# Kernel tuning notes

Hardware: AMD Instinct MI355X
Metric: run time of the kernel (lower is better)

## Reference

```python
import jax, jax.numpy as jnp
import numpy as np

SEQ_LEN = 4096
D_IN = 1024
D_OUT = 1024


def setup_inputs() -> dict:
    key = jax.random.key(0)
    k_x, k_q, k_k, k_v = jax.random.split(key, 4)
    s = 1.0 / np.sqrt(D_IN)
    return {
        "x": jax.random.normal(k_x, (SEQ_LEN, D_IN), dtype=jnp.float32),
        "W_query": jax.random.normal(k_q, (D_IN, D_OUT), dtype=jnp.float32) * s,
        "W_key": jax.random.normal(k_k, (D_IN, D_OUT), dtype=jnp.float32) * s,
        "W_value": jax.random.normal(k_v, (D_IN, D_OUT), dtype=jnp.float32) * s,
    }


def reference(x, W_query, W_key, W_value):
    # QKV projections (Linear without bias): [S, d_out]
    q = x @ W_query
    k = x @ W_key
    v = x @ W_value
    # Full S x S score matrix, causal mask, scaled softmax
    scores = q @ k.T  # [S, S]
    seq_len = x.shape[0]
    causal = jnp.tril(jnp.ones((seq_len, seq_len), dtype=bool))
    scores = jnp.where(causal, scores, -jnp.inf)
    scale = 1.0 / jnp.sqrt(jnp.asarray(k.shape[-1], dtype=scores.dtype))
    attn = jax.nn.softmax(scores * scale, axis=-1)
    return attn @ v  # [S, d_out]
```

## Files before the change

kernel.cpp:

```cpp
#include <hip/hip_runtime.h>
#include <math.h>

#define SEQ 4096
#define DIM 1024

typedef unsigned short u16;
typedef __attribute__((ext_vector_type(8))) short short8;
typedef __attribute__((ext_vector_type(4))) float floatx4;
typedef __attribute__((ext_vector_type(4))) unsigned short us4;

__device__ __forceinline__ float bf2f(u16 u) {
    union { unsigned int i; float f; } c; c.i = ((unsigned int)u) << 16; return c.f;
}
__device__ __forceinline__ u16 f2bf(float f) {
    union { float f; unsigned int i; } c; c.f = f;
    return (u16)((c.i + 0x7fffu + ((c.i >> 16) & 1u)) >> 16);
}
__device__ __forceinline__ void gload_lds16(const u16* g, u16* l) {
    __builtin_amdgcn_global_load_lds((const __attribute__((address_space(1))) void*)g,
                                     (__attribute__((address_space(3))) void*)l, 16, 0, 0);
}

__device__ __forceinline__ void tile64(const u16* __restrict__ A,
                                       const u16* __restrict__ B,
                                       u16 (&As)[3][2048], u16 (&Bs)[3][2048],
                                       int lda, int ldb,
                                       int row0, int col0, int kend,
                                       int wave, int lane,
                                       floatx4 (&acc)[2][2]) {
    const int wm = wave & 1, wn = wave >> 1;
    const int s0 = wave * 64 + lane;
    const int r0 = s0 >> 2, q0 = ((s0 & 3) ^ ((s0 >> 3) & 3)) * 8;
    const u16* aP = A + (size_t)(row0 + r0) * lda + q0;
    const u16* bP = B + (size_t)(col0 + r0) * ldb + q0;
    const int l0 = wave * 512;
    const int frow = lane & 15;
    const int xq = (((lane >> 4) ^ ((frow >> 1) & 3))) * 8;
    const int mrow0 = wm * 32, nrow0 = wn * 32;
    const int niter = kend >> 5;

    gload_lds16(aP, &As[0][l0]); gload_lds16(bP, &Bs[0][l0]); aP += 32; bP += 32;
    gload_lds16(aP, &As[1][l0]); gload_lds16(bP, &Bs[1][l0]); aP += 32; bP += 32;

    int cur = 0, pre = 2;
    for (int it = 0; it < niter - 2; ++it) {
        asm volatile("s_waitcnt vmcnt(2)\n\ts_barrier" ::: "memory");
        short8 af[2], bfr[2];
#pragma unroll
        for (int t = 0; t < 2; ++t) {
            af[t]  = *(const short8*)&As[cur][(mrow0 + t * 16 + frow) * 32 + xq];
            bfr[t] = *(const short8*)&Bs[cur][(nrow0 + t * 16 + frow) * 32 + xq];
        }
        gload_lds16(aP, &As[pre][l0]); gload_lds16(bP, &Bs[pre][l0]);
        aP += 32; bP += 32;
#pragma unroll
        for (int mt = 0; mt < 2; ++mt)
#pragma unroll
            for (int nt = 0; nt < 2; ++nt)
                acc[mt][nt] = __builtin_amdgcn_mfma_f32_16x16x32_bf16(
                    af[mt], bfr[nt], acc[mt][nt], 0, 0, 0);
        cur = (cur == 2) ? 0 : cur + 1;
        pre = (pre == 2) ? 0 : pre + 1;
    }
#pragma unroll
    for (int fin = 0; fin < 2; ++fin) {
        if (fin == 0)
            asm volatile("s_waitcnt vmcnt(2)\n\ts_barrier" ::: "memory");
        else
            asm volatile("s_waitcnt vmcnt(0)\n\ts_barrier" ::: "memory");
        short8 af[2], bfr[2];
#pragma unroll
        for (int t = 0; t < 2; ++t) {
            af[t]  = *(const short8*)&As[cur][(mrow0 + t * 16 + frow) * 32 + xq];
            bfr[t] = *(const short8*)&Bs[cur][(nrow0 + t * 16 + frow) * 32 + xq];
        }
#pragma unroll
        for (int mt = 0; mt < 2; ++mt)
#pragma unroll
            for (int nt = 0; nt < 2; ++nt)
                acc[mt][nt] = __builtin_amdgcn_mfma_f32_16x16x32_bf16(
                    af[mt], bfr[nt], acc[mt][nt], 0, 0, 0);
        cur = (cur == 2) ? 0 : cur + 1;
    }
}

__global__ __launch_bounds__(256) void gemm128(const u16* __restrict__ A,
                                               const u16* __restrict__ B,
                                               u16* __restrict__ Cout,
                                               u16* __restrict__ VtOut,
                                               int lda, int ldb, int ldc, int Kdim,
                                               float scale0) {
    const int row0 = blockIdx.y * 128;
    const int col0 = blockIdx.x * 128;

    __shared__ u16 As[3][4096];
    __shared__ u16 Bs[3][4096];

    const int tid  = threadIdx.x;
    const int wave = tid >> 6;
    const int lane = tid & 63;
    const int wm = wave & 1;
    const int wn = wave >> 1;

    const int s0 = wave * 128 + lane;
    const int s1 = s0 + 64;
    const int r0s = s0 >> 2, q0s = ((s0 & 3) ^ ((s0 >> 3) & 3)) * 8;
    const int r1s = s1 >> 2, q1s = ((s1 & 3) ^ ((s1 >> 3) & 3)) * 8;
    const u16* aP0 = A + (size_t)(row0 + r0s) * lda + q0s;
    const u16* aP1 = A + (size_t)(row0 + r1s) * lda + q1s;
    const u16* bP0 = B + (size_t)(col0 + r0s) * ldb + q0s;
    const u16* bP1 = B + (size_t)(col0 + r1s) * ldb + q1s;
    const int l0 = wave * 1024;

    floatx4 acc[4][4] = {};
    const int niter = Kdim >> 5;
    const int frow = lane & 15;
    const int xq = (((lane >> 4) ^ ((frow >> 1) & 3))) * 8;

    auto stage = [&](int c) {
        gload_lds16(aP0, &As[c][l0]);
        gload_lds16(aP1, &As[c][l0 + 512]);
        gload_lds16(bP0, &Bs[c][l0]);
        gload_lds16(bP1, &Bs[c][l0 + 512]);
        aP0 += 32; aP1 += 32; bP0 += 32; bP1 += 32;
    };
    stage(0);
    stage(1);

    auto compute_tile = [&](int c) {
        short8 af[4], bfr[4];
#pragma unroll
        for (int t = 0; t < 4; ++t) {
            af[t]  = *(const short8*)&As[c][(wm * 64 + t * 16 + frow) * 32 + xq];
            bfr[t] = *(const short8*)&Bs[c][(wn * 64 + t * 16 + frow) * 32 + xq];
        }
#pragma unroll
        for (int mt = 0; mt < 4; ++mt)
#pragma unroll
            for (int nt = 0; nt < 4; ++nt)
                acc[mt][nt] = __builtin_amdgcn_mfma_f32_16x16x32_bf16(
                    af[mt], bfr[nt], acc[mt][nt], 0, 0, 0);
    };

    int cur = 0, pre = 2;
    for (int it = 0; it < niter - 2; ++it) {
        asm volatile("s_waitcnt vmcnt(4)\n\ts_barrier" ::: "memory");
        short8 af[4], bfr[4];
#pragma unroll
        for (int t = 0; t < 4; ++t) {
            af[t]  = *(const short8*)&As[cur][(wm * 64 + t * 16 + frow) * 32 + xq];
            bfr[t] = *(const short8*)&Bs[cur][(wn * 64 + t * 16 + frow) * 32 + xq];
        }
        stage(pre);
#pragma unroll
        for (int mt = 0; mt < 4; ++mt)
#pragma unroll
            for (int nt = 0; nt < 4; ++nt)
                acc[mt][nt] = __builtin_amdgcn_mfma_f32_16x16x32_bf16(
                    af[mt], bfr[nt], acc[mt][nt], 0, 0, 0);
        cur = (cur == 2) ? 0 : cur + 1;
        pre = (pre == 2) ? 0 : pre + 1;
    }
    asm volatile("s_waitcnt vmcnt(4)\n\ts_barrier" ::: "memory");
    compute_tile(cur);
    cur = (cur == 2) ? 0 : cur + 1;
    asm volatile("s_waitcnt vmcnt(0)\n\ts_barrier" ::: "memory");
    compute_tile(cur);

    const int cr = (lane >> 4) * 4;
    const int cc = lane & 15;
    if (col0 >= 2048) {
#pragma unroll
        for (int mt = 0; mt < 4; ++mt)
#pragma unroll
            for (int nt = 0; nt < 4; ++nt) {
                const int row = row0 + wm * 64 + mt * 16 + cr;
                const int col = (col0 - 2048) + wn * 64 + nt * 16 + cc;
                us4 o = { f2bf(acc[mt][nt][0]), f2bf(acc[mt][nt][1]),
                          f2bf(acc[mt][nt][2]), f2bf(acc[mt][nt][3]) };
                *(us4*)&VtOut[(size_t)col * SEQ + row] = o;
            }
    } else {
        const float sc = (col0 < 1024) ? scale0 : 1.0f;
#pragma unroll
        for (int mt = 0; mt < 4; ++mt)
#pragma unroll
            for (int nt = 0; nt < 4; ++nt)
#pragma unroll
                for (int r = 0; r < 4; ++r) {
                    const int row = row0 + wm * 64 + mt * 16 + cr + r;
                    const int col = col0 + wn * 64 + nt * 16 + cc;
                    Cout[(size_t)row * ldc + col] = f2bf(acc[mt][nt][r] * sc);
                }
    }
}

__global__ __launch_bounds__(256) void scores64(const u16* __restrict__ QK,
                                                u16* __restrict__ E,
                                                float* __restrict__ Lsum) {
    const int t = blockIdx.x;
    int by = (int)((sqrtf(8.0f * t + 1.0f) - 1.0f) * 0.5f);
    while ((by + 1) * (by + 2) / 2 <= t) ++by;
    while (by * (by + 1) / 2 > t) --by;
    const int bx = t - by * (by + 1) / 2;
    const int row0 = by * 64, col0 = bx * 64;

    __shared__ u16 As[3][2048], Bs[3][2048];
    const int tid = threadIdx.x, wave = tid >> 6, lane = tid & 63;

    floatx4 acc[2][2] = {};
    tile64(QK, QK + 1024, As, Bs, 2048, 2048, row0, col0, DIM, wave, lane, acc);

    const int wm = wave & 1, wn = wave >> 1;
    const int cr = (lane >> 4) * 4, cc = lane & 15;
#pragma unroll
    for (int mt = 0; mt < 2; ++mt) {
#pragma unroll
        for (int r = 0; r < 4; ++r) {
            const int grow = row0 + wm * 32 + mt * 16 + cr + r;
            float rowsum = 0.f;
#pragma unroll
            for (int nt = 0; nt < 2; ++nt) {
                const int gcol = col0 + wn * 32 + nt * 16 + cc;
                const float e = (gcol <= grow) ? __expf(acc[mt][nt][r]) : 0.f;
                rowsum += e;
                E[(size_t)grow * SEQ + gcol] = f2bf(e);
            }
            rowsum += __shfl_xor(rowsum, 1);
            rowsum += __shfl_xor(rowsum, 2);
            rowsum += __shfl_xor(rowsum, 4);
            rowsum += __shfl_xor(rowsum, 8);
            if (cc == 0) atomicAdd(&Lsum[grow], rowsum);
        }
    }
}

__global__ __launch_bounds__(256) void pv64(const u16* __restrict__ E,
                                            const u16* __restrict__ Vt,
                                            float* __restrict__ O,
                                            const float* __restrict__ Lsum,
                                            unsigned* __restrict__ Tick) {
    __shared__ u16 As[3][2048], Bs[3][2048];
    __shared__ unsigned sh_t;
    const int tid = threadIdx.x, wave = tid >> 6, lane = tid & 63;
    const int wm = wave & 1, wn = wave >> 1;
    const int cr = (lane >> 4) * 4, cc = lane & 15;

    for (;;) {
        if (tid == 0) sh_t = atomicAdd(Tick, 1u);
        __syncthreads();
        const unsigned t = sh_t;
        if (t >= 1024u) return;
        const int r = 63 - (int)(t >> 4);
        const int x = (int)(t & 15u);
        const int row0 = r * 64, col0 = x * 64;

        floatx4 acc[2][2] = {};
        tile64(E, Vt, As, Bs, SEQ, SEQ, row0, col0, row0 + 64, wave, lane, acc);

#pragma unroll
        for (int mt = 0; mt < 2; ++mt)
#pragma unroll
            for (int rr = 0; rr < 4; ++rr) {
                const int grow = row0 + wm * 32 + mt * 16 + cr + rr;
                const float invl = __builtin_amdgcn_rcpf(Lsum[grow]);
#pragma unroll
                for (int nt = 0; nt < 2; ++nt) {
                    const int col = col0 + wn * 32 + nt * 16 + cc;
                    O[(size_t)grow * DIM + col] = acc[mt][nt][rr] * invl;
                }
            }
    }
}

__global__ __launch_bounds__(256) void prep(const float* __restrict__ x,
                                            const float* __restrict__ W0,
                                            const float* __restrict__ W1,
                                            const float* __restrict__ W2,
                                            u16* __restrict__ xb,
                                            u16* __restrict__ Wt,
                                            float* __restrict__ Lsum,
                                            unsigned* __restrict__ Tick) {
    __shared__ float tile[32][33];
    const int b = blockIdx.x;
    const int tid = threadIdx.x;
    if (b < 4096) {
        const size_t i = ((size_t)b * 256 + tid) * 4;
        const float4 v = *(const float4*)(x + i);
        us4 o = { f2bf(v.x), f2bf(v.y), f2bf(v.z), f2bf(v.w) };
        *(us4*)(xb + i) = o;
    } else if (b < 7168) {
        const int t = b - 4096;
        const int z = t >> 10;
        const int idx = t & 1023;
        const float* W = (z == 0) ? W0 : (z == 1) ? W1 : W2;
        u16* out = Wt + (size_t)z * DIM * DIM;
        const int bx = (idx & 31) * 32;
        const int by = (idx >> 5) * 32;
        const int tx = tid & 31;
        const int ty = (tid >> 5) * 4;
#pragma unroll
        for (int r = 0; r < 4; ++r)
            tile[ty + r][tx] = W[(size_t)(by + ty + r) * DIM + bx + tx];
        __syncthreads();
#pragma unroll
        for (int r = 0; r < 4; ++r)
            out[(size_t)(bx + ty + r) * DIM + by + tx] = f2bf(tile[tx][ty + r]);
    } else {
        const int t = b - 7168;
        *(float4*)(Lsum + (size_t)(t * 256 + tid) * 4) =
            make_float4(0.f, 0.f, 0.f, 0.f);
        if (t == 0 && tid == 0) *Tick = 0u;
    }
}

extern "C" void kernel_launch(void* const* d_in, const int* in_sizes, int n_in,
                              void* d_out, int out_size, void* d_ws, size_t ws_size,
                              hipStream_t stream) {
    const float* x  = (const float*)d_in[0];
    const float* Wq = (const float*)d_in[1];
    const float* Wk = (const float*)d_in[2];
    const float* Wv = (const float*)d_in[3];

    u16* xb    = (u16*)d_ws;
    u16* Wt    = xb  + (size_t)SEQ * DIM;
    u16* QK    = Wt  + (size_t)3072 * DIM;
    u16* Vt    = QK  + (size_t)SEQ * 2048;
    u16* E     = Vt  + (size_t)DIM * SEQ;
    float* Lsum = (float*)(E + (size_t)SEQ * SEQ);
    unsigned* Tick = (unsigned*)(Lsum + SEQ);

    prep<<<7172, 256, 0, stream>>>(x, Wq, Wk, Wv, xb, Wt, Lsum, Tick);

    gemm128<<<dim3(24, 32), 256, 0, stream>>>(
        xb, Wt, QK, Vt, DIM, DIM, 2048, DIM, 0.03125f);

    scores64<<<2080, 256, 0, stream>>>(QK, E, Lsum);

    pv64<<<768, 256, 0, stream>>>(E, Vt, (float*)d_out, Lsum, Tick);
}
```

Before: 220.9 us.

## Split V projection into scores kernel, use 128 score tiles, static PV schedule

Q/K projection now runs alone, and the V projection is merged into the scores kernel so the two run side by side. Score tiles grow from 64 to 128 (528 causal tiles instead of 2080), which improves data reuse. The PV kernel drops its atomic work-stealing ticket for a fixed interleaved mapping that pairs heavy and light rows. The risks are load imbalance from the static schedule and fewer, larger blocks in the scores stage.

```diff
diff --git a/kernel.cpp b/kernel.cpp
--- a/kernel.cpp
+++ b/kernel.cpp
@@ -21,87 +21,13 @@
                                      (__attribute__((address_space(3))) void*)l, 16, 0, 0);
 }
 
-__device__ __forceinline__ void tile64(const u16* __restrict__ A,
-                                       const u16* __restrict__ B,
-                                       u16 (&As)[3][2048], u16 (&Bs)[3][2048],
-                                       int lda, int ldb,
-                                       int row0, int col0, int kend,
-                                       int wave, int lane,
-                                       floatx4 (&acc)[2][2]) {
+__device__ __forceinline__ void pipe128(const u16* __restrict__ A,
+                                        const u16* __restrict__ B,
+                                        u16 (&As)[3][4096], u16 (&Bs)[3][4096],
+                                        int lda, int ldb, int row0, int col0,
+                                        int wave, int lane,
+                                        floatx4 (&acc)[4][4]) {
     const int wm = wave & 1, wn = wave >> 1;
-    const int s0 = wave * 64 + lane;
-    const int r0 = s0 >> 2, q0 = ((s0 & 3) ^ ((s0 >> 3) & 3)) * 8;
-    const u16* aP = A + (size_t)(row0 + r0) * lda + q0;
-    const u16* bP = B + (size_t)(col0 + r0) * ldb + q0;
-    const int l0 = wave * 512;
-    const int frow = lane & 15;
-    const int xq = (((lane >> 4) ^ ((frow >> 1) & 3))) * 8;
-    const int mrow0 = wm * 32, nrow0 = wn * 32;
-    const int niter = kend >> 5;
-
-    gload_lds16(aP, &As[0][l0]); gload_lds16(bP, &Bs[0][l0]); aP += 32; bP += 32;
-    gload_lds16(aP, &As[1][l0]); gload_lds16(bP, &Bs[1][l0]); aP += 32; bP += 32;
-
-    int cur = 0, pre = 2;
-    for (int it = 0; it < niter - 2; ++it) {
-        asm volatile("s_waitcnt vmcnt(2)\n\ts_barrier" ::: "memory");
-        short8 af[2], bfr[2];
-#pragma unroll
-        for (int t = 0; t < 2; ++t) {
-            af[t]  = *(const short8*)&As[cur][(mrow0 + t * 16 + frow) * 32 + xq];
-            bfr[t] = *(const short8*)&Bs[cur][(nrow0 + t * 16 + frow) * 32 + xq];
-        }
-        gload_lds16(aP, &As[pre][l0]); gload_lds16(bP, &Bs[pre][l0]);
-        aP += 32; bP += 32;
-#pragma unroll
-        for (int mt = 0; mt < 2; ++mt)
-#pragma unroll
-            for (int nt = 0; nt < 2; ++nt)
-                acc[mt][nt] = __builtin_amdgcn_mfma_f32_16x16x32_bf16(
-                    af[mt], bfr[nt], acc[mt][nt], 0, 0, 0);
-        cur = (cur == 2) ? 0 : cur + 1;
-        pre = (pre == 2) ? 0 : pre + 1;
-    }
-#pragma unroll
-    for (int fin = 0; fin < 2; ++fin) {
-        if (fin == 0)
-            asm volatile("s_waitcnt vmcnt(2)\n\ts_barrier" ::: "memory");
-        else
-            asm volatile("s_waitcnt vmcnt(0)\n\ts_barrier" ::: "memory");
-        short8 af[2], bfr[2];
-#pragma unroll
-        for (int t = 0; t < 2; ++t) {
-            af[t]  = *(const short8*)&As[cur][(mrow0 + t * 16 + frow) * 32 + xq];
-            bfr[t] = *(const short8*)&Bs[cur][(nrow0 + t * 16 + frow) * 32 + xq];
-        }
-#pragma unroll
-        for (int mt = 0; mt < 2; ++mt)
-#pragma unroll
-            for (int nt = 0; nt < 2; ++nt)
-                acc[mt][nt] = __builtin_amdgcn_mfma_f32_16x16x32_bf16(
-                    af[mt], bfr[nt], acc[mt][nt], 0, 0, 0);
-        cur = (cur == 2) ? 0 : cur + 1;
-    }
-}
-
-__global__ __launch_bounds__(256) void gemm128(const u16* __restrict__ A,
-                                               const u16* __restrict__ B,
-                                               u16* __restrict__ Cout,
-                                               u16* __restrict__ VtOut,
-                                               int lda, int ldb, int ldc, int Kdim,
-                                               float scale0) {
-    const int row0 = blockIdx.y * 128;
-    const int col0 = blockIdx.x * 128;
-
-    __shared__ u16 As[3][4096];
-    __shared__ u16 Bs[3][4096];
-
-    const int tid  = threadIdx.x;
-    const int wave = tid >> 6;
-    const int lane = tid & 63;
-    const int wm = wave & 1;
-    const int wn = wave >> 1;
-
     const int s0 = wave * 128 + lane;
     const int s1 = s0 + 64;
     const int r0s = s0 >> 2, q0s = ((s0 & 3) ^ ((s0 >> 3) & 3)) * 8;
@@ -111,9 +37,6 @@
     const u16* bP0 = B + (size_t)(col0 + r0s) * ldb + q0s;
     const u16* bP1 = B + (size_t)(col0 + r1s) * ldb + q1s;
     const int l0 = wave * 1024;
-
-    floatx4 acc[4][4] = {};
-    const int niter = Kdim >> 5;
     const int frow = lane & 15;
     const int xq = (((lane >> 4) ^ ((frow >> 1) & 3))) * 8;
 
@@ -143,7 +66,7 @@
     };
 
     int cur = 0, pre = 2;
-    for (int it = 0; it < niter - 2; ++it) {
+    for (int it = 0; it < 30; ++it) {
         asm volatile("s_waitcnt vmcnt(4)\n\ts_barrier" ::: "memory");
         short8 af[4], bfr[4];
 #pragma unroll
@@ -166,71 +89,89 @@
     cur = (cur == 2) ? 0 : cur + 1;
     asm volatile("s_waitcnt vmcnt(0)\n\ts_barrier" ::: "memory");
     compute_tile(cur);
-
-    const int cr = (lane >> 4) * 4;
-    const int cc = lane & 15;
-    if (col0 >= 2048) {
+}
+
+__global__ __launch_bounds__(256) void projQK(const u16* __restrict__ xb,
+                                              const u16* __restrict__ Wt,
+                                              u16* __restrict__ QK,
+                                              float scale0) {
+    __shared__ u16 As[3][4096], Bs[3][4096];
+    const int row0 = blockIdx.y * 128;
+    const int col0 = blockIdx.x * 128;
+    const int tid = threadIdx.x, wave = tid >> 6, lane = tid & 63;
+    const int wm = wave & 1, wn = wave >> 1;
+
+    floatx4 acc[4][4] = {};
+    pipe128(xb, Wt, As, Bs, DIM, DIM, row0, col0, wave, lane, acc);
+
+    const int cr = (lane >> 4) * 4, cc = lane & 15;
+    const float sc = (col0 < 1024) ? scale0 : 1.0f;
+#pragma unroll
+    for (int mt = 0; mt < 4; ++mt)
+#pragma unroll
+        for (int nt = 0; nt < 4; ++nt)
+#pragma unroll
+            for (int r = 0; r < 4; ++r) {
+                const int row = row0 + wm * 64 + mt * 16 + cr + r;
+                const int col = col0 + wn * 64 + nt * 16 + cc;
+                QK[(size_t)row * 2048 + col] = f2bf(acc[mt][nt][r] * sc);
+            }
+}
+
+__global__ __launch_bounds__(256) void scoresV(const u16* __restrict__ QK,
+                                               const u16* __restrict__ xb,
+                                               const u16* __restrict__ Wt,
+                                               u16* __restrict__ E,
+                                               u16* __restrict__ Vt,
+                                               float* __restrict__ Lsum) {
+    __shared__ u16 As[3][4096], Bs[3][4096];
+    const int t = blockIdx.x;
+    const int tid = threadIdx.x, wave = tid >> 6, lane = tid & 63;
+    const int wm = wave & 1, wn = wave >> 1;
+    const int cr = (lane >> 4) * 4, cc = lane & 15;
+
+    floatx4 acc[4][4] = {};
+    if (t < 256) {
+        const int row0 = (t >> 3) * 128;
+        const int colv = (t & 7) * 128;
+        pipe128(xb, Wt, As, Bs, DIM, DIM, row0, 2048 + colv, wave, lane, acc);
 #pragma unroll
         for (int mt = 0; mt < 4; ++mt)
 #pragma unroll
             for (int nt = 0; nt < 4; ++nt) {
                 const int row = row0 + wm * 64 + mt * 16 + cr;
-                const int col = (col0 - 2048) + wn * 64 + nt * 16 + cc;
+                const int col = colv + wn * 64 + nt * 16 + cc;
                 us4 o = { f2bf(acc[mt][nt][0]), f2bf(acc[mt][nt][1]),
                           f2bf(acc[mt][nt][2]), f2bf(acc[mt][nt][3]) };
-                *(us4*)&VtOut[(size_t)col * SEQ + row] = o;
+                *(us4*)&Vt[(size_t)col * SEQ + row] = o;
             }
     } else {
-        const float sc = (col0 < 1024) ? scale0 : 1.0f;
-#pragma unroll
-        for (int mt = 0; mt < 4; ++mt)
-#pragma unroll
-            for (int nt = 0; nt < 4; ++nt)
-#pragma unroll
-                for (int r = 0; r < 4; ++r) {
-                    const int row = row0 + wm * 64 + mt * 16 + cr + r;
-                    const int col = col0 + wn * 64 + nt * 16 + cc;
-                    Cout[(size_t)row * ldc + col] = f2bf(acc[mt][nt][r] * sc);
+        const int s = t - 256;
+        int by = (int)((sqrtf(8.0f * s + 1.0f) - 1.0f) * 0.5f);
+        while ((by + 1) * (by + 2) / 2 <= s) ++by;
+        while (by * (by + 1) / 2 > s) --by;
+        const int bx = s - by * (by + 1) / 2;
+        const int row0 = by * 128, col0 = bx * 128;
+        pipe128(QK, QK + 1024, As, Bs, 2048, 2048, row0, col0, wave, lane, acc);
+#pragma unroll
+        for (int mt = 0; mt < 4; ++mt) {
+#pragma unroll
+            for (int r = 0; r < 4; ++r) {
+                const int grow = row0 + wm * 64 + mt * 16 + cr + r;
+                float rowsum = 0.f;
+#pragma unroll
+                for (int nt = 0; nt < 4; ++nt) {
+                    const int gcol = col0 + wn * 64 + nt * 16 + cc;
+                    const float e = (gcol <= grow) ? __expf(acc[mt][nt][r]) : 0.f;
+                    rowsum += e;
+                    E[(size_t)grow * SEQ + gcol] = f2bf(e);
                 }
-    }
-}
-
-__global__ __launch_bounds__(256) void scores64(const u16* __restrict__ QK,
-                                                u16* __restrict__ E,
-                                                float* __restrict__ Lsum) {
-    const int t = blockIdx.x;
-    int by = (int)((sqrtf(8.0f * t + 1.0f) - 1.0f) * 0.5f);
-    while ((by + 1) * (by + 2) / 2 <= t) ++by;
-    while (by * (by + 1) / 2 > t) --by;
-    const int bx = t - by * (by + 1) / 2;
-    const int row0 = by * 64, col0 = bx * 64;
-
-    __shared__ u16 As[3][2048], Bs[3][2048];
-    const int tid = threadIdx.x, wave = tid >> 6, lane = tid & 63;
-
-    floatx4 acc[2][2] = {};
-    tile64(QK, QK + 1024, As, Bs, 2048, 2048, row0, col0, DIM, wave, lane, acc);
-
-    const int wm = wave & 1, wn = wave >> 1;
-    const int cr = (lane >> 4) * 4, cc = lane & 15;
-#pragma unroll
-    for (int mt = 0; mt < 2; ++mt) {
-#pragma unroll
-        for (int r = 0; r < 4; ++r) {
-            const int grow = row0 + wm * 32 + mt * 16 + cr + r;
-            float rowsum = 0.f;
-#pragma unroll
-            for (int nt = 0; nt < 2; ++nt) {
-                const int gcol = col0 + wn * 32 + nt * 16 + cc;
-                const float e = (gcol <= grow) ? __expf(acc[mt][nt][r]) : 0.f;
-                rowsum += e;
-                E[(size_t)grow * SEQ + gcol] = f2bf(e);
+                rowsum += __shfl_xor(rowsum, 1);
+                rowsum += __shfl_xor(rowsum, 2);
+                rowsum += __shfl_xor(rowsum, 4);
+                rowsum += __shfl_xor(rowsum, 8);
+                if (cc == 0) atomicAdd(&Lsum[grow], rowsum);
             }
-            rowsum += __shfl_xor(rowsum, 1);
-            rowsum += __shfl_xor(rowsum, 2);
-            rowsum += __shfl_xor(rowsum, 4);
-            rowsum += __shfl_xor(rowsum, 8);
-            if (cc == 0) atomicAdd(&Lsum[grow], rowsum);
         }
     }
 }
@@ -238,39 +179,101 @@
 __global__ __launch_bounds__(256) void pv64(const u16* __restrict__ E,
                                             const u16* __restrict__ Vt,
                                             float* __restrict__ O,
-                                            const float* __restrict__ Lsum,
-                                            unsigned* __restrict__ Tick) {
+                                            const float* __restrict__ Lsum) {
+    const int lin = blockIdx.x + (blockIdx.y << 4);
+    const int c = lin & 7;
+    const int j = lin >> 3;
+    const int x = j & 15;
+    const int m = j >> 4;
+    const unsigned long long PK = 0x2F3F20301F0F1000ULL;
+    const int base = (int)((PK >> (m * 8)) & 0x3F);
+    const int r = base + ((m & 2) ? -c : c);
+    const int row0 = r * 64;
+    const int col0 = x * 64;
+    const int kend = row0 + 64;
+
     __shared__ u16 As[3][2048], Bs[3][2048];
-    __shared__ unsigned sh_t;
-    const int tid = threadIdx.x, wave = tid >> 6, lane = tid & 63;
-    const int wm = wave & 1, wn = wave >> 1;
+
+    const int tid  = threadIdx.x;
+    const int wave = tid >> 6;
+    const int lane = tid & 63;
+    const int wm = wave & 1;
+    const int wn = wave >> 1;
+
+    const int s0 = wave * 64 + lane;
+    const int r0 = s0 >> 2, q0 = ((s0 & 3) ^ ((s0 >> 3) & 3)) * 8;
+    const u16* aP = E  + (size_t)(row0 + r0) * SEQ + q0;
+    const u16* bP = Vt + (size_t)(col0 + r0) * SEQ + q0;
+    const int l0 = wave * 512;
+
+    floatx4 acc[2][2] = {};
+    const int niter = kend >> 5;
+    const int frow = lane & 15;
+    const int xq = (((lane >> 4) ^ ((frow >> 1) & 3))) * 8;
+    const int mrow0 = wm * 32, nrow0 = wn * 32;
+
+    auto stage = [&](int cb) {
+        gload_lds16(aP, &As[cb][l0]);
+        gload_lds16(bP, &Bs[cb][l0]);
+        aP += 32; bP += 32;
+    };
+    stage(0);
+    stage(1);
+
+    auto compute_tile = [&](int cb) {
+        short8 af[2], bfr[2];
+#pragma unroll
+        for (int t = 0; t < 2; ++t) {
+            af[t]  = *(const short8*)&As[cb][(mrow0 + t * 16 + frow) * 32 + xq];
+            bfr[t] = *(const short8*)&Bs[cb][(nrow0 + t * 16 + frow) * 32 + xq];
+        }
+#pragma unroll
+        for (int mt = 0; mt < 2; ++mt)
+#pragma unroll
+            for (int nt = 0; nt < 2; ++nt)
+                acc[mt][nt] = __builtin_amdgcn_mfma_f32_16x16x32_bf16(
+                    af[mt], bfr[nt], acc[mt][nt], 0, 0, 0);
+    };
+
+    int cur = 0, pre = 2;
+    for (int it = 0; it < niter - 2; ++it) {
+        asm volatile("s_waitcnt vmcnt(2)\n\ts_barrier" ::: "memory");
+        short8 af[2], bfr[2];
+#pragma unroll
+        for (int t = 0; t < 2; ++t) {
+            af[t]  = *(const short8*)&As[cur][(mrow0 + t * 16 + frow) * 32 + xq];
+            bfr[t] = *(const short8*)&Bs[cur][(nrow0 + t * 16 + frow) * 32 + xq];
+        }
+        stage(pre);
+#pragma unroll
+        for (int mt = 0; mt < 2; ++mt)
+#pragma unroll
+            for (int nt = 0; nt < 2; ++nt)
+                acc[mt][nt] = __builtin_amdgcn_mfma_f32_16x16x32_bf16(
+                    af[mt], bfr[nt], acc[mt][nt], 0, 0, 0);
+        cur = (cur == 2) ? 0 : cur + 1;
+        pre = (pre == 2) ? 0 : pre + 1;
+    }
+    asm volatile("s_waitcnt vmcnt(2)\n\ts_barrier" ::: "memory");
+    compute_tile(cur);
+    cur = (cur == 2) ? 0 : cur + 1;
+    asm volatile("s_waitcnt vmcnt(0)\n\ts_barrier" ::: "memory");
+    compute_tile(cur);
+
+    float* Oo = O;
     const int cr = (lane >> 4) * 4, cc = lane & 15;
-
-    for (;;) {
-        if (tid == 0) sh_t = atomicAdd(Tick, 1u);
-        __syncthreads();
-        const unsigned t = sh_t;
-        if (t >= 1024u) return;
-        const int r = 63 - (int)(t >> 4);
-        const int x = (int)(t & 15u);
-        const int row0 = r * 64, col0 = x * 64;
-
-        floatx4 acc[2][2] = {};
-        tile64(E, Vt, As, Bs, SEQ, SEQ, row0, col0, row0 + 64, wave, lane, acc);
-
-#pragma unroll
-        for (int mt = 0; mt < 2; ++mt)
-#pragma unroll
-            for (int rr = 0; rr < 4; ++rr) {
-                const int grow = row0 + wm * 32 + mt * 16 + cr + rr;
-                const float invl = __builtin_amdgcn_rcpf(Lsum[grow]);
-#pragma unroll
-                for (int nt = 0; nt < 2; ++nt) {
-                    const int col = col0 + wn * 32 + nt * 16 + cc;
-                    O[(size_t)grow * DIM + col] = acc[mt][nt][rr] * invl;
-                }
+#pragma unroll
+    for (int mt = 0; mt < 2; ++mt)
+#pragma unroll
+        for (int rr = 0; rr < 4; ++rr) {
+            const int grow = row0 + wm * 32 + mt * 16 + cr + rr;
+            const float invl = __builtin_amdgcn_rcpf(Lsum[grow]);
+#pragma unroll
+            for (int nt = 0; nt < 2; ++nt) {
+                const int col = col0 + wn * 32 + nt * 16 + cc;
+                Oo[(size_t)grow * DIM + col] = acc[mt][nt][rr] * invl;
             }
-    }
+        }
 }
 
 __global__ __launch_bounds__(256) void prep(const float* __restrict__ x,
@@ -279,8 +282,7 @@
                                             const float* __restrict__ W2,
                                             u16* __restrict__ xb,
                                             u16* __restrict__ Wt,
-                                            float* __restrict__ Lsum,
-                                            unsigned* __restrict__ Tick) {
+                                            float* __restrict__ Lsum) {
     __shared__ float tile[32][33];
     const int b = blockIdx.x;
     const int tid = threadIdx.x;
@@ -310,7 +312,6 @@
         const int t = b - 7168;
         *(float4*)(Lsum + (size_t)(t * 256 + tid) * 4) =
             make_float4(0.f, 0.f, 0.f, 0.f);
-        if (t == 0 && tid == 0) *Tick = 0u;
     }
 }
 
@@ -328,14 +329,12 @@
     u16* Vt    = QK  + (size_t)SEQ * 2048;
     u16* E     = Vt  + (size_t)DIM * SEQ;
     float* Lsum = (float*)(E + (size_t)SEQ * SEQ);
-    unsigned* Tick = (unsigned*)(Lsum + SEQ);
-
-    prep<<<7172, 256, 0, stream>>>(x, Wq, Wk, Wv, xb, Wt, Lsum, Tick);
-
-    gemm128<<<dim3(24, 32), 256, 0, stream>>>(
-        xb, Wt, QK, Vt, DIM, DIM, 2048, DIM, 0.03125f);
-
-    scores64<<<2080, 256, 0, stream>>>(QK, E, Lsum);
-
-    pv64<<<768, 256, 0, stream>>>(E, Vt, (float*)d_out, Lsum, Tick);
-}
+
+    prep<<<7172, 256, 0, stream>>>(x, Wq, Wk, Wv, xb, Wt, Lsum);
+
+    projQK<<<dim3(16, 32), 256, 0, stream>>>(xb, Wt, QK, 0.03125f);
+
+    scoresV<<<784, 256, 0, stream>>>(QK, xb, Wt, E, Vt, Lsum);
+
+    pv64<<<dim3(16, 64), 256, 0, stream>>>(E, Vt, (float*)d_out, Lsum);
+}
```

New measurement: 192.2 us. -13.0%, faster.
